# Optimization experiments

Hardware: AMD Instinct MI355X
Metric: run time of the kernel (lower is better)

The kernel has to match this reference:

```python
import jax, jax.numpy as jnp
import numpy as np

DE_NEIGHBORS = 3
DEPTH = 2


def square_distance(src, dst):
    # src: [B, N, 3], dst: [B, S, 3] -> pairwise squared L2 [B, N, S]
    return (jnp.sum(src * src, axis=-1)[:, :, None]
            + jnp.sum(dst * dst, axis=-1)[:, None, :]
            - 2.0 * jnp.einsum('bnc,bsc->bns', src, dst))


def propagate(xyz1, xyz2, points1, points2):
    # xyz1: [B, N, 3] fine coords; xyz2: [B, S, 3] coarse coords
    # points1: [B, C1, N] skip feats; points2: [B, C2, S] coarse feats
    pts2 = points2.transpose(0, 2, 1)  # [B, S, C2]
    dists = square_distance(xyz1, xyz2)  # [B, N, S]
    neg_d, idx = jax.lax.top_k(-dists, DE_NEIGHBORS)  # smallest-k distances
    d = -neg_d  # [B, N, K]
    w = 1.0 / (d + 1e-8)
    w = w / jnp.sum(w, axis=-1, keepdims=True)  # [B, N, K]
    # gather neighbor features: [B, N, K, C2]
    gathered = jax.vmap(lambda p, i: p[i])(pts2, idx)
    interp = jnp.sum(gathered * w[..., None], axis=2)  # [B, N, C2]
    m = interp.mean()
    s = jnp.std(interp - m, ddof=1)  # torch.std default is unbiased
    interp = (interp - m) / (s + 1e-5)
    new_points = jnp.concatenate([points1.transpose(0, 2, 1), interp], axis=-1)
    return new_points.transpose(0, 2, 1)  # [B, C1+C2, N]


def setup_inputs() -> dict:
    key = jax.random.key(0)
    ks = jax.random.split(key, 6)
    B = 8
    return {
        'xyz0': jax.random.normal(ks[0], (B, 8192, 3), jnp.float32),
        'xyz1': jax.random.normal(ks[1], (B, 2048, 3), jnp.float32),
        'xyz2': jax.random.normal(ks[2], (B, 512, 3), jnp.float32),
        'x0': jax.random.normal(ks[3], (B, 128, 8192), jnp.float32),
        'x1': jax.random.normal(ks[4], (B, 256, 2048), jnp.float32),
        'x2': jax.random.normal(ks[5], (B, 512, 512), jnp.float32),
    }


def reference(xyz0, xyz1, xyz2, x0, x1, x2):
    # forward reverses the lists: index 0 = coarsest level
    xyz_list = [xyz2, xyz1, xyz0]
    x_list = [x2, x1, x0]
    x = x_list[0]
    for i in range(DEPTH):
        x = propagate(xyz_list[i + 1], xyz_list[i], x_list[i + 1], x)
    return x  # [8, 128+256+512, 8192]
```

## Files before the change

kernel.cpp:

```cpp
#include <hip/hip_runtime.h>
#include <cstdint>
#include <math.h>


__device__ __forceinline__ void dev_merge6(const float* __restrict__ cd,
                                           const int* __restrict__ ci,
                                           int& o0, int& o1, int& o2,
                                           float& w0, float& w1, float& w2) {
    float d0 = 1e30f, d1 = 1e30f, d2 = 1e30f;
    int j0 = 0, j1 = 0, j2 = 0;
#pragma unroll
    for (int k = 0; k < 6; ++k) {
        const float d = cd[k];
        const int s = ci[k];
        const bool lt0 = d < d0, lt1 = d < d1, lt2 = d < d2;
        d2 = lt1 ? d1 : (lt2 ? d : d2);
        j2 = lt1 ? j1 : (lt2 ? s : j2);
        d1 = lt0 ? d0 : (lt1 ? d : d1);
        j1 = lt0 ? j0 : (lt1 ? s : j1);
        d0 = lt0 ? d : d0;
        j0 = lt0 ? s : j0;
    }
    const float a = 1.0f / (d0 + 1e-8f);
    const float b = 1.0f / (d1 + 1e-8f);
    const float c = 1.0f / (d2 + 1e-8f);
    const float ws = (a + b) + c;
    o0 = j0; o1 = j1; o2 = j2;
    w0 = a / ws; w1 = b / ws; w2 = c / ws;
}

template <int CHUNK>
__device__ __forceinline__ void dev_knn_lds(const float* __restrict__ fine,
                                            const float* __restrict__ coarse,
                                            int N, int S, int nch,
                                            int b, int nb, int chunk, int tid,
                                            float4* __restrict__ lc,
                                            float* __restrict__ cand_d,
                                            int* __restrict__ cand_i) {
#pragma clang fp contract(off)
    const int s0 = chunk * CHUNK;
    const float* cb = coarse + ((size_t)b * S + s0) * 3;
    for (int s = tid; s < CHUNK; s += 256) {
        const float x = cb[3 * s], y = cb[3 * s + 1], z = cb[3 * s + 2];
        lc[s] = make_float4(x, y, z, (x * x + y * y) + z * z);
    }
    __syncthreads();
    const int n = nb * 256 + tid;
    const float* fp = fine + ((size_t)b * N + n) * 3;
    const float px = fp[0], py = fp[1], pz = fp[2];
    const float psq = (px * px + py * py) + pz * pz;
    float d0 = 1e30f, d1 = 1e30f, d2 = 1e30f;
    int i0 = 0, i1 = 0, i2 = 0;
#pragma unroll 8
    for (int s = 0; s < CHUNK; ++s) {
        const float4 c = lc[s];
        const float dot = (px * c.x + py * c.y) + pz * c.z;
        const float d = fmaf(-2.0f, dot, psq + c.w);
        if (__any(d < d2)) {
            const bool lt0 = d < d0, lt1 = d < d1, lt2 = d < d2;
            d2 = lt1 ? d1 : (lt2 ? d : d2);
            i2 = lt1 ? i1 : (lt2 ? s : i2);
            d1 = lt0 ? d0 : (lt1 ? d : d1);
            i1 = lt0 ? i0 : (lt1 ? s : i1);
            d0 = lt0 ? d : d0;
            i0 = lt0 ? s : i0;
        }
    }
    const size_t p = (((size_t)b * N + n) * nch + chunk) * 3;
    cand_d[p] = d0; cand_d[p + 1] = d1; cand_d[p + 2] = d2;
    cand_i[p] = s0 + i0; cand_i[p + 1] = s0 + i1; cand_i[p + 2] = s0 + i2;
}

__device__ __forceinline__ void dev_transpose(const float* __restrict__ in,
                                              float* __restrict__ out,
                                              int C, long in_bs, long out_bs, int out_rs,
                                              int b, int rt, int ct, int tid,
                                              float* __restrict__ tile ) {
    const int r0 = rt * 32, c0 = ct * 32;
    const float* inb = in + (size_t)b * in_bs;
    float* outb = out + (size_t)b * out_bs;
    const int tx = tid & 31, ty = tid >> 5;
#pragma unroll
    for (int i = 0; i < 32; i += 8) {
        tile[(ty + i) * 33 + tx] = inb[(size_t)(r0 + ty + i) * C + (c0 + tx)];
    }
    __syncthreads();
#pragma unroll
    for (int i = 0; i < 32; i += 8) {
        outb[(size_t)(c0 + ty + i) * out_rs + (r0 + tx)] = tile[tx * 33 + (ty + i)];
    }
}

__global__ __launch_bounds__(256) void k_front(const float* __restrict__ xyz0,
                                               const float* __restrict__ xyz1,
                                               const float* __restrict__ xyz2,
                                               const float* __restrict__ x0,
                                               const float* __restrict__ x1,
                                               const float* __restrict__ x2,
                                               float* __restrict__ pts1,
                                               float* __restrict__ inter,
                                               float* __restrict__ out,
                                               float* __restrict__ cand_d2,
                                               int* __restrict__ cand_i2,
                                               float* __restrict__ cand_d1,
                                               int* __restrict__ cand_i1) {
    __shared__ __align__(16) char smem[16384];
    const int id = blockIdx.x;
    const int tid = threadIdx.x;
    if (id < 512) {
        dev_knn_lds<1024>(xyz0, xyz1, 8192, 2048, 2,
                          id >> 6, id & 31, (id >> 5) & 1, tid,
                          (float4*)smem, cand_d2, cand_i2);
    } else if (id < 640) {
        const int t = id - 512;
        dev_knn_lds<256>(xyz1, xyz2, 2048, 512, 2,
                         t >> 4, t & 7, (t >> 3) & 1, tid,
                         (float4*)smem, cand_d1, cand_i1);
    } else if (id < 8832) {
        const size_t i = (size_t)(id - 640) * 256 + tid;
        const size_t b = i >> 18;
        const size_t off = i & (((size_t)1 << 18) - 1);
        const float4* src = (const float4*)(x0 + b * (size_t)128 * 8192);
        float4* dst = (float4*)(out + b * (size_t)896 * 8192);
        dst[off] = src[off];
    } else if (id < 12928) {
        const int t = id - 8832;
        const int ct = t & 63, rt = (t >> 6) & 7, b = t >> 9;
        dev_transpose(x1, inter, 2048, 256 * 2048, (long)2048 * 768, 768,
                      b, rt, ct, tid, (float*)smem);
    } else {
        const int t = id - 12928;
        const int ct = t & 15, rt = (t >> 4) & 15, b = t >> 8;
        dev_transpose(x2, pts1, 512, 512 * 512, 512 * 512, 512,
                      b, rt, ct, tid, (float*)smem);
    }
}

__global__ __launch_bounds__(256) void k_interp1_fused(const float* __restrict__ pts,
                                                       const float* __restrict__ cand_d,
                                                       const int* __restrict__ cand_i,
                                                       float* __restrict__ inter,
                                                       double* __restrict__ partials1) {
    __shared__ int   si[16][3];
    __shared__ float sw[16][3];
    const int b = blockIdx.x, nb = blockIdx.y;
    const int n0 = nb * 16;
    const int tid = threadIdx.x;
    if (tid < 16) {
        const size_t pt = (size_t)b * 2048 + n0 + tid;
        dev_merge6(cand_d + pt * 6, cand_i + pt * 6,
                   si[tid][0], si[tid][1], si[tid][2],
                   sw[tid][0], sw[tid][1], sw[tid][2]);
    }
    __syncthreads();
    const float4* pb4 = (const float4*)(pts + (size_t)b * 512 * 512);
    const int pg = tid >> 6, f = tid & 63;
    double ls = 0.0, lq = 0.0;
#pragma unroll
    for (int g = 0; g < 4; ++g) {
        const int pl = g * 4 + pg;
        const size_t p = (size_t)b * 2048 + n0 + pl;
        const size_t r0 = (size_t)si[pl][0] * 128;
        const size_t r1 = (size_t)si[pl][1] * 128;
        const size_t r2 = (size_t)si[pl][2] * 128;
        const float w0 = sw[pl][0], w1 = sw[pl][1], w2 = sw[pl][2];
        float4* out4 = (float4*)(inter + p * 768 + 256);
#pragma unroll
        for (int k = 0; k < 2; ++k) {
            const int c = f + k * 64;
            const float4 a = pb4[r0 + c], d = pb4[r1 + c], e = pb4[r2 + c];
            float4 v;
            v.x = (w0 * a.x + w1 * d.x) + w2 * e.x;
            v.y = (w0 * a.y + w1 * d.y) + w2 * e.y;
            v.z = (w0 * a.z + w1 * d.z) + w2 * e.z;
            v.w = (w0 * a.w + w1 * d.w) + w2 * e.w;
            out4[c] = v;
            ls += (double)v.x + (double)v.y + (double)v.z + (double)v.w;
            lq += (double)v.x * v.x + (double)v.y * v.y
                + (double)v.z * v.z + (double)v.w * v.w;
        }
    }
    __shared__ double sa[256], sb[256];
    sa[tid] = ls; sb[tid] = lq; __syncthreads();
    for (int s = 128; s > 0; s >>= 1) {
        if (tid < s) { sa[tid] += sa[tid + s]; sb[tid] += sb[tid + s]; }
        __syncthreads();
    }
    if (tid == 0) {
        const size_t pl = (size_t)b * gridDim.y + nb;
        partials1[2 * pl] = sa[0]; partials1[2 * pl + 1] = sb[0];
    }
}

__global__ __launch_bounds__(256) void k_interp_stats(const float* __restrict__ pts,
                                                      const float* __restrict__ cand_d,
                                                      const int* __restrict__ cand_i,
                                                      int N, int S, int C,
                                                      double* __restrict__ partials) {
    __shared__ int   si[32][3];
    __shared__ float sw[32][3];
    const int b = blockIdx.x, nb = blockIdx.y, cb = blockIdx.z;
    const int n0 = nb * 32;
    const int tid = threadIdx.x;
    if (tid < 32) {
        const size_t pt = (size_t)b * N + n0 + tid;
        dev_merge6(cand_d + pt * 6, cand_i + pt * 6,
                   si[tid][0], si[tid][1], si[tid][2],
                   sw[tid][0], sw[tid][1], sw[tid][2]);
    }
    __syncthreads();
    const int C4 = C >> 2;
    const float4* pbf = (const float4*)(pts + (size_t)b * S * C) + (cb * 64);
    const int f = tid & 63;
    const int pg = tid >> 6;
    double ls = 0.0, lq = 0.0;
#pragma unroll
    for (int g = 0; g < 8; ++g) {
        const int nl = g * 4 + pg;
        const size_t r0 = (size_t)si[nl][0] * C4;
        const size_t r1 = (size_t)si[nl][1] * C4;
        const size_t r2 = (size_t)si[nl][2] * C4;
        const float w0 = sw[nl][0], w1 = sw[nl][1], w2 = sw[nl][2];
        const float4 a = pbf[r0 + f], c = pbf[r1 + f], e = pbf[r2 + f];
        const float vx = (w0 * a.x + w1 * c.x) + w2 * e.x;
        const float vy = (w0 * a.y + w1 * c.y) + w2 * e.y;
        const float vz = (w0 * a.z + w1 * c.z) + w2 * e.z;
        const float vw = (w0 * a.w + w1 * c.w) + w2 * e.w;
        ls += (double)vx + (double)vy + (double)vz + (double)vw;
        lq += (double)vx * vx + (double)vy * vy + (double)vz * vz + (double)vw * vw;
    }
    __shared__ double sa[256], sb[256];
    sa[tid] = ls; sb[tid] = lq; __syncthreads();
    for (int s = 128; s > 0; s >>= 1) {
        if (tid < s) { sa[tid] += sa[tid + s]; sb[tid] += sb[tid + s]; }
        __syncthreads();
    }
    if (tid == 0) {
        const size_t pl = ((size_t)cb * gridDim.x + b) * gridDim.y + nb;
        partials[2 * pl] = sa[0]; partials[2 * pl + 1] = sb[0];
    }
}

__global__ __launch_bounds__(256) void k_fin_combined(const double* __restrict__ partials1,
                                                      int P1,
                                                      const double* __restrict__ partials2,
                                                      int P2, int P2lo,
                                                      float* __restrict__ stats4) {
    __shared__ double red[6][256];
    const int t = threadIdx.x;
    double s1 = 0.0, q1 = 0.0, s2l = 0.0, q2l = 0.0, s2h = 0.0, q2h = 0.0;
    for (int i = t; i < P1; i += 256) { s1 += partials1[2 * i]; q1 += partials1[2 * i + 1]; }
    for (int i = t; i < P2; i += 256) {
        const double s = partials2[2 * i], q = partials2[2 * i + 1];
        if (i < P2lo) { s2l += s; q2l += q; } else { s2h += s; q2h += q; }
    }
    red[0][t] = s1; red[1][t] = q1; red[2][t] = s2l;
    red[3][t] = q2l; red[4][t] = s2h; red[5][t] = q2h;
    __syncthreads();
    for (int s = 128; s > 0; s >>= 1) {
        if (t < s) {
#pragma unroll
            for (int r = 0; r < 6; ++r) red[r][t] += red[r][t + s];
        }
        __syncthreads();
    }
    if (t == 0) {
        const double nelem1 = 8388608.0;
        const double cnt2   = 50331648.0;
        const double cnthi  = 33554432.0;
        const double S1 = red[0][0], Q1 = red[1][0];
        const double m1 = S1 / nelem1;
        const double v1 = (Q1 - S1 * S1 / nelem1) / (nelem1 - 1.0);
        const double sd1 = sqrt(v1 > 0.0 ? v1 : 0.0);
        const float rs1f = (float)(1.0 / (sd1 + 1e-5));
        const float m1f = (float)m1;
        const double a1 = (double)rs1f;
        const double b1 = -(double)m1f * (double)rs1f;
        const double S2l = red[2][0], Q2l = red[3][0];
        const double S2h = red[4][0], Q2h = red[5][0];
        const double Sf = S2l + a1 * S2h + b1 * cnthi;
        const double Qf = Q2l + a1 * a1 * Q2h + 2.0 * a1 * b1 * S2h + b1 * b1 * cnthi;
        const double m2 = Sf / cnt2;
        const double v2 = (Qf - Sf * Sf / cnt2) / (cnt2 - 1.0);
        const double sd2 = sqrt(v2 > 0.0 ? v2 : 0.0);
        const double rs2 = 1.0 / (sd2 + 1e-5);
        stats4[0] = (float)rs2;
        stats4[1] = (float)(-m2 * rs2);
        stats4[2] = (float)(a1 * rs2);
        stats4[3] = (float)((b1 - m2) * rs2);
    }
}

__global__ __launch_bounds__(256) void k_interp2_write(const float* __restrict__ pts,
                                                       const float* __restrict__ cand_d,
                                                       const int* __restrict__ cand_i,
                                                       const float* __restrict__ stats4,
                                                       float* __restrict__ out) {
    __shared__ float tile[64][65];
    __shared__ int   si[64][3];
    __shared__ float sw[64][3];
    const int b = blockIdx.x, nt = blockIdx.y, cc = blockIdx.z;
    const float alpha = (cc < 4) ? stats4[0] : stats4[2];
    const float beta  = (cc < 4) ? stats4[1] : stats4[3];
    const int n0 = nt * 64, c0 = cc * 64;
    const int tid = threadIdx.x;
    if (tid < 64) {
        const size_t pt = (size_t)b * 8192 + n0 + tid;
        dev_merge6(cand_d + pt * 6, cand_i + pt * 6,
                   si[tid][0], si[tid][1], si[tid][2],
                   sw[tid][0], sw[tid][1], sw[tid][2]);
    }
    __syncthreads();
    const float* pb = pts + (size_t)b * 2048 * 768 + c0;
    const int cl = tid & 63;
    const int pg = tid >> 6;
#pragma unroll
    for (int pass = 0; pass < 16; ++pass) {
        const int nl = pass * 4 + pg;
        const float v = (sw[nl][0] * pb[(size_t)si[nl][0] * 768 + cl]
                       + sw[nl][1] * pb[(size_t)si[nl][1] * 768 + cl])
                       + sw[nl][2] * pb[(size_t)si[nl][2] * 768 + cl];
        tile[nl][cl] = alpha * v + beta;
    }
    __syncthreads();
    float* ob = out + (size_t)b * 896 * 8192 + (size_t)(128 + c0) * 8192 + n0;
    const int tn = tid & 63, tc0 = tid >> 6;
#pragma unroll
    for (int pass = 0; pass < 16; ++pass) {
        const int tc = pass * 4 + tc0;
        ob[(size_t)tc * 8192 + tn] = tile[tn][tc];
    }
}

extern "C" void kernel_launch(void* const* d_in, const int* in_sizes, int n_in,
                              void* d_out, int out_size, void* d_ws, size_t ws_size,
                              hipStream_t stream) {
    const float* xyz0 = (const float*)d_in[0];
    const float* xyz1 = (const float*)d_in[1];
    const float* xyz2 = (const float*)d_in[2];
    const float* x0   = (const float*)d_in[3];
    const float* x1   = (const float*)d_in[4];
    const float* x2   = (const float*)d_in[5];
    float* out = (float*)d_out;
    char* ws = (char*)d_ws;

    size_t off = 0;
    auto alloc = [&](size_t bytes) {
        size_t o = off;
        off = (off + bytes + 255) & ~(size_t)255;
        return o;
    };
    float*  stats4    = (float*)(ws + alloc(4 * sizeof(float)));
    double* partials1 = (double*)(ws + alloc((size_t)1024 * 2 * sizeof(double)));
    double* partials2 = (double*)(ws + alloc((size_t)6144 * 2 * sizeof(double)));
    float*  pts1      = (float*)(ws + alloc((size_t)8 * 512 * 512 * 4));
    float*  inter     = (float*)(ws + alloc((size_t)8 * 2048 * 768 * 4));
    float*  cand_d2   = (float*)(ws + alloc((size_t)65536 * 6 * 4));
    int*    cand_i2   = (int*)(ws + alloc((size_t)65536 * 6 * 4));
    float*  cand_d1   = (float*)(ws + alloc((size_t)16384 * 6 * 4));
    int*    cand_i1   = (int*)(ws + alloc((size_t)16384 * 6 * 4));

    k_front<<<14976, 256, 0, stream>>>(xyz0, xyz1, xyz2, x0, x1, x2,
                                       pts1, inter, out,
                                       cand_d2, cand_i2, cand_d1, cand_i1);
    k_interp1_fused<<<dim3(8, 128), 256, 0, stream>>>(
        pts1, cand_d1, cand_i1, inter, partials1);
    k_interp_stats<<<dim3(8, 256, 3), 256, 0, stream>>>(
        inter, cand_d2, cand_i2, 8192, 2048, 768, partials2);
    k_fin_combined<<<1, 256, 0, stream>>>(partials1, 1024, partials2, 6144, 2048, stats4);
    k_interp2_write<<<dim3(8, 128, 12), 256, 0, stream>>>(inter, cand_d2, cand_i2,
                                                          stats4, out);
}
```

Baseline: 188.3 us.

## Process two fine points per thread in KNN and split coarse set into four chunks

The level-2 KNN now has each thread handle two fine points against a 512-point LDS chunk, so each LDS coarse load is reused twice. The coarse set is split into four chunks instead of two, and the merge step now combines 12 candidates. Both KNN loops separate distance computation (8-wide batches) from branch-free top-3 insertion and drop the wave-level __any early-out. The change trades more candidate storage and merge work, and the loss of the skip branch, for better ILP and LDS reuse.

After: 177.4 us. 5.8% less time.

```diff
diff --git a/kernel.cpp b/kernel.cpp
--- a/kernel.cpp
+++ b/kernel.cpp
@@ -3,14 +3,15 @@
 #include <math.h>
 
 
-__device__ __forceinline__ void dev_merge6(const float* __restrict__ cd,
-                                           const int* __restrict__ ci,
-                                           int& o0, int& o1, int& o2,
-                                           float& w0, float& w1, float& w2) {
+template <int NC>
+__device__ __forceinline__ void dev_merge(const float* __restrict__ cd,
+                                          const int* __restrict__ ci,
+                                          int& o0, int& o1, int& o2,
+                                          float& w0, float& w1, float& w2) {
     float d0 = 1e30f, d1 = 1e30f, d2 = 1e30f;
     int j0 = 0, j1 = 0, j2 = 0;
 #pragma unroll
-    for (int k = 0; k < 6; ++k) {
+    for (int k = 0; k < NC; ++k) {
         const float d = cd[k];
         const int s = ci[k];
         const bool lt0 = d < d0, lt1 = d < d1, lt2 = d < d2;
@@ -29,14 +30,26 @@
     w0 = a / ws; w1 = b / ws; w2 = c / ws;
 }
 
+__device__ __forceinline__ void dev_ins3(float d, int s,
+                                         float& d0, float& d1, float& d2,
+                                         int& i0, int& i1, int& i2) {
+    const bool lt0 = d < d0, lt1 = d < d1, lt2 = d < d2;
+    d2 = lt1 ? d1 : (lt2 ? d : d2);
+    i2 = lt1 ? i1 : (lt2 ? s : i2);
+    d1 = lt0 ? d0 : (lt1 ? d : d1);
+    i1 = lt0 ? i0 : (lt1 ? s : i1);
+    d0 = lt0 ? d : d0;
+    i0 = lt0 ? s : i0;
+}
+
 template <int CHUNK>
-__device__ __forceinline__ void dev_knn_lds(const float* __restrict__ fine,
-                                            const float* __restrict__ coarse,
-                                            int N, int S, int nch,
-                                            int b, int nb, int chunk, int tid,
-                                            float4* __restrict__ lc,
-                                            float* __restrict__ cand_d,
-                                            int* __restrict__ cand_i) {
+__device__ __forceinline__ void dev_knn2pt(const float* __restrict__ fine,
+                                           const float* __restrict__ coarse,
+                                           int N, int S, int nch,
+                                           int b, int nb, int chunk, int tid,
+                                           float4* __restrict__ lc,
+                                           float* __restrict__ cand_d,
+                                           int* __restrict__ cand_i) {
 #pragma clang fp contract(off)
     const int s0 = chunk * CHUNK;
     const float* cb = coarse + ((size_t)b * S + s0) * 3;
@@ -45,25 +58,72 @@
         lc[s] = make_float4(x, y, z, (x * x + y * y) + z * z);
     }
     __syncthreads();
+    const int na = nb * 512 + tid;
+    const int nB = na + 256;
+    const float* fa = fine + ((size_t)b * N + na) * 3;
+    const float* fb = fine + ((size_t)b * N + nB) * 3;
+    const float ax = fa[0], ay = fa[1], az = fa[2];
+    const float bx = fb[0], by = fb[1], bz = fb[2];
+    const float asq = (ax * ax + ay * ay) + az * az;
+    const float bsq = (bx * bx + by * by) + bz * bz;
+    float da0 = 1e30f, da1 = 1e30f, da2 = 1e30f;
+    float db0 = 1e30f, db1 = 1e30f, db2 = 1e30f;
+    int ia0 = 0, ia1 = 0, ia2 = 0;
+    int ib0 = 0, ib1 = 0, ib2 = 0;
+    for (int s8 = 0; s8 < CHUNK; s8 += 8) {
+        float dA[8], dB[8];
+#pragma unroll
+        for (int u = 0; u < 8; ++u) {
+            const float4 c = lc[s8 + u];
+            dA[u] = fmaf(-2.0f, (ax * c.x + ay * c.y) + az * c.z, asq + c.w);
+            dB[u] = fmaf(-2.0f, (bx * c.x + by * c.y) + bz * c.z, bsq + c.w);
+        }
+#pragma unroll
+        for (int u = 0; u < 8; ++u) {
+            dev_ins3(dA[u], s8 + u, da0, da1, da2, ia0, ia1, ia2);
+            dev_ins3(dB[u], s8 + u, db0, db1, db2, ib0, ib1, ib2);
+        }
+    }
+    const size_t pa = (((size_t)b * N + na) * nch + chunk) * 3;
+    cand_d[pa] = da0; cand_d[pa + 1] = da1; cand_d[pa + 2] = da2;
+    cand_i[pa] = s0 + ia0; cand_i[pa + 1] = s0 + ia1; cand_i[pa + 2] = s0 + ia2;
+    const size_t pb = (((size_t)b * N + nB) * nch + chunk) * 3;
+    cand_d[pb] = db0; cand_d[pb + 1] = db1; cand_d[pb + 2] = db2;
+    cand_i[pb] = s0 + ib0; cand_i[pb + 1] = s0 + ib1; cand_i[pb + 2] = s0 + ib2;
+}
+
+template <int CHUNK>
+__device__ __forceinline__ void dev_knn1pt(const float* __restrict__ fine,
+                                           const float* __restrict__ coarse,
+                                           int N, int S, int nch,
+                                           int b, int nb, int chunk, int tid,
+                                           float4* __restrict__ lc,
+                                           float* __restrict__ cand_d,
+                                           int* __restrict__ cand_i) {
+#pragma clang fp contract(off)
+    const int s0 = chunk * CHUNK;
+    const float* cb = coarse + ((size_t)b * S + s0) * 3;
+    for (int s = tid; s < CHUNK; s += 256) {
+        const float x = cb[3 * s], y = cb[3 * s + 1], z = cb[3 * s + 2];
+        lc[s] = make_float4(x, y, z, (x * x + y * y) + z * z);
+    }
+    __syncthreads();
     const int n = nb * 256 + tid;
     const float* fp = fine + ((size_t)b * N + n) * 3;
     const float px = fp[0], py = fp[1], pz = fp[2];
     const float psq = (px * px + py * py) + pz * pz;
     float d0 = 1e30f, d1 = 1e30f, d2 = 1e30f;
     int i0 = 0, i1 = 0, i2 = 0;
-#pragma unroll 8
-    for (int s = 0; s < CHUNK; ++s) {
-        const float4 c = lc[s];
-        const float dot = (px * c.x + py * c.y) + pz * c.z;
-        const float d = fmaf(-2.0f, dot, psq + c.w);
-        if (__any(d < d2)) {
-            const bool lt0 = d < d0, lt1 = d < d1, lt2 = d < d2;
-            d2 = lt1 ? d1 : (lt2 ? d : d2);
-            i2 = lt1 ? i1 : (lt2 ? s : i2);
-            d1 = lt0 ? d0 : (lt1 ? d : d1);
-            i1 = lt0 ? i0 : (lt1 ? s : i1);
-            d0 = lt0 ? d : d0;
-            i0 = lt0 ? s : i0;
+    for (int s8 = 0; s8 < CHUNK; s8 += 8) {
+        float dv[8];
+#pragma unroll
+        for (int u = 0; u < 8; ++u) {
+            const float4 c = lc[s8 + u];
+            dv[u] = fmaf(-2.0f, (px * c.x + py * c.y) + pz * c.z, psq + c.w);
+        }
+#pragma unroll
+        for (int u = 0; u < 8; ++u) {
+            dev_ins3(dv[u], s8 + u, d0, d1, d2, i0, i1, i2);
         }
     }
     const size_t p = (((size_t)b * N + n) * nch + chunk) * 3;
@@ -104,18 +164,18 @@
                                                int* __restrict__ cand_i2,
                                                float* __restrict__ cand_d1,
                                                int* __restrict__ cand_i1) {
-    __shared__ __align__(16) char smem[16384];
+    __shared__ __align__(16) char smem[8192];
     const int id = blockIdx.x;
     const int tid = threadIdx.x;
     if (id < 512) {
-        dev_knn_lds<1024>(xyz0, xyz1, 8192, 2048, 2,
-                          id >> 6, id & 31, (id >> 5) & 1, tid,
-                          (float4*)smem, cand_d2, cand_i2);
+        dev_knn2pt<512>(xyz0, xyz1, 8192, 2048, 4,
+                        id >> 6, id & 15, (id >> 4) & 3, tid,
+                        (float4*)smem, cand_d2, cand_i2);
     } else if (id < 640) {
         const int t = id - 512;
-        dev_knn_lds<256>(xyz1, xyz2, 2048, 512, 2,
-                         t >> 4, t & 7, (t >> 3) & 1, tid,
-                         (float4*)smem, cand_d1, cand_i1);
+        dev_knn1pt<256>(xyz1, xyz2, 2048, 512, 2,
+                        t >> 4, t & 7, (t >> 3) & 1, tid,
+                        (float4*)smem, cand_d1, cand_i1);
     } else if (id < 8832) {
         const size_t i = (size_t)(id - 640) * 256 + tid;
         const size_t b = i >> 18;
@@ -148,9 +208,9 @@
     const int tid = threadIdx.x;
     if (tid < 16) {
         const size_t pt = (size_t)b * 2048 + n0 + tid;
-        dev_merge6(cand_d + pt * 6, cand_i + pt * 6,
-                   si[tid][0], si[tid][1], si[tid][2],
-                   sw[tid][0], sw[tid][1], sw[tid][2]);
+        dev_merge<6>(cand_d + pt * 6, cand_i + pt * 6,
+                     si[tid][0], si[tid][1], si[tid][2],
+                     sw[tid][0], sw[tid][1], sw[tid][2]);
     }
     __syncthreads();
     const float4* pb4 = (const float4*)(pts + (size_t)b * 512 * 512);
@@ -204,9 +264,9 @@
     const int tid = threadIdx.x;
     if (tid < 32) {
         const size_t pt = (size_t)b * N + n0 + tid;
-        dev_merge6(cand_d + pt * 6, cand_i + pt * 6,
-                   si[tid][0], si[tid][1], si[tid][2],
-                   sw[tid][0], sw[tid][1], sw[tid][2]);
+        dev_merge<12>(cand_d + pt * 12, cand_i + pt * 12,
+                      si[tid][0], si[tid][1], si[tid][2],
+                      sw[tid][0], sw[tid][1], sw[tid][2]);
     }
     __syncthreads();
     const int C4 = C >> 2;
@@ -306,9 +366,9 @@
     const int tid = threadIdx.x;
     if (tid < 64) {
         const size_t pt = (size_t)b * 8192 + n0 + tid;
-        dev_merge6(cand_d + pt * 6, cand_i + pt * 6,
-                   si[tid][0], si[tid][1], si[tid][2],
-                   sw[tid][0], sw[tid][1], sw[tid][2]);
+        dev_merge<12>(cand_d + pt * 12, cand_i + pt * 12,
+                      si[tid][0], si[tid][1], si[tid][2],
+                      sw[tid][0], sw[tid][1], sw[tid][2]);
     }
     __syncthreads();
     const float* pb = pts + (size_t)b * 2048 * 768 + c0;
@@ -355,8 +415,8 @@
     double* partials2 = (double*)(ws + alloc((size_t)6144 * 2 * sizeof(double)));
     float*  pts1      = (float*)(ws + alloc((size_t)8 * 512 * 512 * 4));
     float*  inter     = (float*)(ws + alloc((size_t)8 * 2048 * 768 * 4));
-    float*  cand_d2   = (float*)(ws + alloc((size_t)65536 * 6 * 4));
-    int*    cand_i2   = (int*)(ws + alloc((size_t)65536 * 6 * 4));
+    float*  cand_d2   = (float*)(ws + alloc((size_t)65536 * 12 * 4));
+    int*    cand_i2   = (int*)(ws + alloc((size_t)65536 * 12 * 4));
     float*  cand_d1   = (float*)(ws + alloc((size_t)16384 * 6 * 4));
     int*    cand_i1   = (int*)(ws + alloc((size_t)16384 * 6 * 4));
 
```
